# Performance work log

Hardware: AMD Instinct MI355X
Metric: run time of the kernel (lower is better)

## Reference

```python
import math
import jax, jax.numpy as jnp
import numpy as np

D_MODEL = 768
N_HEADS = 12
D_K = 64
D_V = 64
LN_EPS = 1e-5


def setup_inputs() -> dict:
    key = jax.random.key(0)
    ks = jax.random.split(key, 12)
    B, S = 4, 2048
    Q = jax.random.normal(ks[0], (B, S, D_MODEL), dtype=jnp.float32)
    K = jax.random.normal(ks[1], (B, S, D_MODEL), dtype=jnp.float32)
    V = jax.random.normal(ks[2], (B, S, D_MODEL), dtype=jnp.float32)
    attn_mask = jax.random.randint(ks[3], (B, S, S), 0, 2).astype(bool)
    sc = 1.0 / math.sqrt(D_MODEL)
    WQ = jax.random.normal(ks[4], (D_MODEL, N_HEADS * D_K), dtype=jnp.float32) * sc
    WK = jax.random.normal(ks[5], (D_MODEL, N_HEADS * D_K), dtype=jnp.float32) * sc
    WV = jax.random.normal(ks[6], (D_MODEL, N_HEADS * D_V), dtype=jnp.float32) * sc
    Wfc = jax.random.normal(ks[7], (N_HEADS * D_V, D_MODEL), dtype=jnp.float32) * sc
    bQ = jnp.zeros((N_HEADS * D_K,), jnp.float32)
    bK = jnp.zeros((N_HEADS * D_K,), jnp.float32)
    bV = jnp.zeros((N_HEADS * D_V,), jnp.float32)
    bfc = jnp.zeros((D_MODEL,), jnp.float32)
    gamma = jnp.ones((D_MODEL,), jnp.float32)
    beta = jnp.zeros((D_MODEL,), jnp.float32)
    return {"Q": Q, "K": K, "V": V, "attn_mask": attn_mask,
            "WQ": WQ, "bQ": bQ, "WK": WK, "bK": bK, "WV": WV, "bV": bV,
            "Wfc": Wfc, "bfc": bfc, "gamma": gamma, "beta": beta}


def reference(Q, K, V, attn_mask, WQ, bQ, WK, bK, WV, bV, Wfc, bfc, gamma, beta):
    B, S, _ = Q.shape
    # projections -> [B, H, S, d]
    q = (Q @ WQ + bQ).reshape(B, S, N_HEADS, D_K).transpose(0, 2, 1, 3)
    k = (K @ WK + bK).reshape(B, S, N_HEADS, D_K).transpose(0, 2, 1, 3)
    v = (V @ WV + bV).reshape(B, S, N_HEADS, D_V).transpose(0, 2, 1, 3)
    # manual scaled dot-product attention with masked_fill(-1e9)
    scores = jnp.einsum('bhqd,bhkd->bhqk', q, k) / math.sqrt(D_K)
    scores = jnp.where(attn_mask[:, None, :, :], jnp.float32(-1e9), scores)
    attn = jax.nn.softmax(scores, axis=-1)
    context = jnp.einsum('bhqk,bhkd->bhqd', attn, v)
    context = context.transpose(0, 2, 1, 3).reshape(B, S, N_HEADS * D_V)
    out = context @ Wfc + bfc + Q  # residual is Q
    # LayerNorm over d_model
    mu = jnp.mean(out, axis=-1, keepdims=True)
    var = jnp.mean((out - mu) ** 2, axis=-1, keepdims=True)
    return (out - mu) * jax.lax.rsqrt(var + LN_EPS) * gamma + beta
```

## Files before the change

### kernel.cpp

```cpp
#include <hip/hip_runtime.h>
#include <stdint.h>

#define DM   768
#define HEADS 12
#define DK    64
#define SEQ  2048
#define BATCH  4

typedef __bf16 bf16_t;
typedef __bf16 bf16x8 __attribute__((ext_vector_type(8)));
typedef __bf16 bf16x4 __attribute__((ext_vector_type(4)));
typedef float  f32x4  __attribute__((ext_vector_type(4)));
typedef float  f32x16 __attribute__((ext_vector_type(16)));
typedef unsigned u32x4 __attribute__((ext_vector_type(4)));

#define LOG2E 1.44269504f
#define MASKVAL (-1.442695e9f)
#define DEFER_THR 8.0f

#define OFF_FLAG 0
#define OFF_MASK 256
#define SZ_MASK  (BATCH*SEQ*(SEQ/32)*4)
#define OFF_WT   (OFF_MASK + SZ_MASK)
#define SZ_WT1   (DM*DM*2)
#define OFF_XB   (OFF_WT + 4*SZ_WT1)
#define SZ_X     (BATCH*SEQ*DM*2)
#define OFF_QP   (OFF_XB + 3*SZ_X)
#define SZ_PROJ  (BATCH*HEADS*SEQ*DK*2)
#define OFF_KP   (OFF_QP + SZ_PROJ)
#define OFF_VT   (OFF_KP + SZ_PROJ)

__device__ __forceinline__ void gload_lds16(const bf16_t* g, bf16_t* l) {
    __builtin_amdgcn_global_load_lds((const __attribute__((address_space(1))) unsigned int*)g,
                                     (__attribute__((address_space(3))) unsigned int*)l, 16, 0, 0);
}

__device__ __forceinline__ unsigned pack2(float lo, float hi) {
    union { bf16_t b[2]; unsigned u; } x;
    x.b[0] = (bf16_t)lo; x.b[1] = (bf16_t)hi;
    return x.u;
}

__global__ void detect_mask_kernel(const unsigned char* __restrict__ m, int* flag) {
    int u = threadIdx.x;
    int any = m[4*u+1] | m[4*u+2] | m[4*u+3];
    unsigned long long b = __ballot(any != 0);
    if (u == 0) *flag = (b == 0ULL) ? 1 : 0;
}

__global__ void pack_mask_kernel(const void* __restrict__ mraw, const int* __restrict__ flag,
                                 unsigned int* __restrict__ words) {
    const unsigned int total = BATCH*SEQ*SEQ;
    const int is32 = *flag;
    const int* mi = (const int*)mraw;
    const unsigned char* mb = (const unsigned char*)mraw;
    unsigned int stride = gridDim.x * blockDim.x;
    unsigned int lane = threadIdx.x & 63u;
    for (unsigned int e = blockIdx.x * blockDim.x + threadIdx.x; e < total; e += stride) {
        int v = is32 ? (mi[e] != 0) : (mb[e] != 0);
        unsigned long long bal = __ballot(v);
        if ((lane & 31u) == 0u)
            words[e >> 5] = (unsigned int)(bal >> ((lane >> 5) * 32u));
    }
}

__global__ void wt_cvt_kernel(const float* __restrict__ W0, const float* __restrict__ W1,
                              const float* __restrict__ W2, const float* __restrict__ W3,
                              bf16_t* __restrict__ dst) {
    const float* W = blockIdx.z == 0 ? W0 : blockIdx.z == 1 ? W1 : blockIdx.z == 2 ? W2 : W3;
    bf16_t* out = dst + (size_t)blockIdx.z * DM * DM;
    __shared__ float tile[64][65];
    int w = threadIdx.x >> 6, u = threadIdx.x & 63;
    int kb = blockIdx.x * 64, nb = blockIdx.y * 64;
    #pragma unroll
    for (int i = 0; i < 16; i++)
        tile[w + 4*i][u] = W[(size_t)(kb + w + 4*i)*DM + nb + u];
    __syncthreads();
    #pragma unroll
    for (int i = 0; i < 16; i++)
        out[(size_t)(nb + w + 4*i)*DM + kb + u] = (bf16_t)tile[u][w + 4*i];
}

__global__ void xcvt_kernel(const float* __restrict__ Q, const float* __restrict__ K,
                            const float* __restrict__ V, bf16_t* __restrict__ XB) {
    int z = blockIdx.y;
    const float* src = z == 0 ? Q : z == 1 ? K : V;
    bf16_t* dst = XB + (size_t)z * BATCH*SEQ*DM;
    size_t i = ((size_t)blockIdx.x * blockDim.x + threadIdx.x) * 8;
    float4 a = *(const float4*)(src + i);
    float4 b = *(const float4*)(src + i + 4);
    bf16x8 o;
    o[0]=(bf16_t)a.x; o[1]=(bf16_t)a.y; o[2]=(bf16_t)a.z; o[3]=(bf16_t)a.w;
    o[4]=(bf16_t)b.x; o[5]=(bf16_t)b.y; o[6]=(bf16_t)b.z; o[7]=(bf16_t)b.w;
    *(bf16x8*)(dst + i) = o;
}

__device__ __forceinline__ void mm_mainloop(const bf16_t* __restrict__ Aptr,
                                            const bf16_t* __restrict__ Bptr,
                                            bf16_t* As, bf16_t* Bs,
                                            f32x4 acc[4][4], int bm, int bn) {
    int tid = threadIdx.x, w = tid >> 6, u = tid & 63, c = u & 15, g = u >> 4;
    int wr = w >> 1, wc = w & 1;
    for (int k0 = 0; k0 < DM; k0 += 64) {
        #pragma unroll
        for (int i = 0; i < 4; i++) {
            int q = i*256 + tid;
            int row = q >> 3, col8 = q & 7;
            gload_lds16(Aptr + (size_t)(bm*128 + row)*DM + k0 + col8*8, As + (i*256 + w*64)*8);
            gload_lds16(Bptr + (size_t)(bn*128 + row)*DM + k0 + col8*8, Bs + (i*256 + w*64)*8);
        }
        __syncthreads();
        #pragma unroll
        for (int kk = 0; kk < 2; kk++) {
            bf16x8 a[4], bfr[4];
            #pragma unroll
            for (int mi = 0; mi < 4; mi++)
                a[mi] = *(const bf16x8*)(As + (wr*64 + mi*16 + c)*64 + kk*32 + g*8);
            #pragma unroll
            for (int ni = 0; ni < 4; ni++)
                bfr[ni] = *(const bf16x8*)(Bs + (wc*64 + ni*16 + c)*64 + kk*32 + g*8);
            #pragma unroll
            for (int mi = 0; mi < 4; mi++)
                #pragma unroll
                for (int ni = 0; ni < 4; ni++)
                    acc[mi][ni] = __builtin_amdgcn_mfma_f32_16x16x32_bf16(a[mi], bfr[ni], acc[mi][ni], 0, 0, 0);
        }
        __syncthreads();
    }
}

__global__ __launch_bounds__(256) void proj128_kernel(
        const bf16_t* __restrict__ XB, const bf16_t* __restrict__ WT,
        const float* __restrict__ bQ, const float* __restrict__ bK, const float* __restrict__ bV,
        bf16_t* __restrict__ QP, bf16_t* __restrict__ KP, bf16_t* __restrict__ VT) {
    int z = blockIdx.z;
    const bf16_t* Aptr = XB + (size_t)z * BATCH*SEQ*DM;
    const bf16_t* Bptr = WT + (size_t)z * DM * DM;
    const float* bias = z == 0 ? bQ : z == 1 ? bK : bV;
    float scale = (z == 0) ? 0.125f * LOG2E : 1.0f;
    __shared__ __align__(16) bf16_t As[128*64], Bs[128*64];
    int tid = threadIdx.x, w = tid >> 6, u = tid & 63, c = u & 15, g = u >> 4;
    int wr = w >> 1, wc = w & 1;
    int bm = blockIdx.x, bn = blockIdx.y;
    f32x4 zero = {0.f,0.f,0.f,0.f};
    f32x4 acc[4][4] = {{zero,zero,zero,zero},{zero,zero,zero,zero},
                       {zero,zero,zero,zero},{zero,zero,zero,zero}};
    mm_mainloop(Aptr, Bptr, As, Bs, acc, bm, bn);
    int h = bn*2 + wc;
    #pragma unroll
    for (int ni = 0; ni < 4; ni++) {
        int d = ni*16 + c;
        float bv = bias[h*64 + d];
        if (z < 2) {
            bf16_t* dst = (z == 0) ? QP : KP;
            #pragma unroll
            for (int mi = 0; mi < 4; mi++)
                #pragma unroll
                for (int j = 0; j < 4; j++) {
                    int r = bm*128 + wr*64 + mi*16 + 4*g + j;
                    int bidx = r >> 11, s = r & 2047;
                    dst[(((size_t)bidx*HEADS + h)*SEQ + s)*DK + d] = (bf16_t)((acc[mi][ni][j] + bv)*scale);
                }
        } else {
            #pragma unroll
            for (int mi = 0; mi < 4; mi++) {
                bf16x4 pk;
                #pragma unroll
                for (int j = 0; j < 4; j++) pk[j] = (bf16_t)(acc[mi][ni][j] + bv);
                int r0 = bm*128 + wr*64 + mi*16 + 4*g;
                int bidx = r0 >> 11, s0 = r0 & 2047;
                *(bf16x4*)(VT + (((size_t)bidx*HEADS + h)*DK + d)*SEQ + s0) = pk;
            }
        }
    }
}

__global__ __launch_bounds__(256) void out128_kernel(
        const bf16_t* __restrict__ CTX, const bf16_t* __restrict__ WfcT,
        const float* __restrict__ bfc, const float* __restrict__ Qres, float* __restrict__ out) {
    __shared__ __align__(16) bf16_t As[128*64], Bs[128*64];
    int tid = threadIdx.x, w = tid >> 6, u = tid & 63, c = u & 15, g = u >> 4;
    int wr = w >> 1, wc = w & 1;
    int bm = blockIdx.x, bn = blockIdx.y;
    f32x4 zero = {0.f,0.f,0.f,0.f};
    f32x4 acc[4][4] = {{zero,zero,zero,zero},{zero,zero,zero,zero},
                       {zero,zero,zero,zero},{zero,zero,zero,zero}};
    mm_mainloop(CTX, WfcT, As, Bs, acc, bm, bn);
    #pragma unroll
    for (int ni = 0; ni < 4; ni++) {
        int n = bn*128 + wc*64 + ni*16 + c;
        float bv = bfc[n];
        #pragma unroll
        for (int mi = 0; mi < 4; mi++)
            #pragma unroll
            for (int j = 0; j < 4; j++) {
                int r = bm*128 + wr*64 + mi*16 + 4*g + j;
                out[(size_t)r*DM + n] = acc[mi][ni][j] + bv + Qres[(size_t)r*DM + n];
            }
    }
}

__global__ __launch_bounds__(256) void attn_kernel(
        const bf16_t* __restrict__ QP, const bf16_t* __restrict__ KP, const bf16_t* __restrict__ VT,
        const unsigned int* __restrict__ maskw, bf16_t* __restrict__ CTX) {
    __shared__ __align__(16) bf16_t kbuf[2][64*64];
    __shared__ __align__(16) bf16_t vbuf[2][64*64];
    __shared__ __align__(16) float lut4[64];
    int tid = threadIdx.x, w = tid >> 6, u = tid & 63;
    int qc = u & 31, hi = u >> 5;
    int b = blockIdx.z, h = blockIdx.y;
    int qg = blockIdx.x * 128 + w * 32 + qc;
    size_t bh = (size_t)(b * HEADS + h);
    const bf16_t* qp = QP + bh * SEQ * DK;
    const bf16_t* kp = KP + bh * SEQ * DK;
    const bf16_t* vt = VT + bh * DK * SEQ;
    const unsigned int* mwq = maskw + ((size_t)b * SEQ + qg) * (SEQ/32);

    if (tid < 64) lut4[tid] = (((tid >> 2) >> (tid & 3)) & 1) ? MASKVAL : 0.f;

    bf16x8 qf[4];
    #pragma unroll
    for (int t = 0; t < 4; t++)
        qf[t] = *(const bf16x8*)(qp + (size_t)qg*DK + 16*t + 8*hi);

    int sr = tid >> 3, scc = tid & 7;

    f32x16 zz = {0,0,0,0,0,0,0,0,0,0,0,0,0,0,0,0};
    f32x16 acc0 = zz, acc1 = zz;
    float mrun = -3e38f, lsum = 0.f;

    #pragma unroll
    for (int i = 0; i < 2; i++) {
        int r = i*32 + sr;
        int gc = (scc ^ (r & 7)) << 3;
        gload_lds16(kp + (size_t)r*DK + gc,       &kbuf[0][0] + i*2048 + tid*8);
        gload_lds16(vt + (size_t)r*SEQ + 0 + gc,  &vbuf[0][0] + i*2048 + tid*8);
    }
    uint2 mv = *(const uint2*)(mwq);
    __syncthreads();

    for (int kt = 0; kt < SEQ/64; kt++) {
        int kb = kt * 64;
        int cur = kt & 1;
        uint2 mv_next;
        if (kt + 1 < SEQ/64) {
            mv_next = *(const uint2*)(mwq + ((kb + 64) >> 5));
            int nkb = kb + 64;
            #pragma unroll
            for (int i = 0; i < 2; i++) {
                int r = i*32 + sr;
                int gc = (scc ^ (r & 7)) << 3;
                gload_lds16(kp + (size_t)(nkb + r)*DK + gc, &kbuf[cur^1][0] + i*2048 + tid*8);
                gload_lds16(vt + (size_t)r*SEQ + nkb + gc,  &vbuf[cur^1][0] + i*2048 + tid*8);
            }
        }
        const bf16_t* kl = &kbuf[cur][0];
        const bf16_t* vl = &vbuf[cur][0];

        f32x4 am0[4], am1[4];
        #pragma unroll
        for (int j = 0; j < 4; j++) {
            am0[j] = *(const f32x4*)&lut4[((mv.x >> (8*j + 4*hi)) & 0xFu) * 4];
            am1[j] = *(const f32x4*)&lut4[((mv.y >> (8*j + 4*hi)) & 0xFu) * 4];
        }

        f32x16 s0 = zz, s1 = zz;
        __builtin_amdgcn_s_setprio(1);
        #pragma unroll
        for (int t = 0; t < 4; t++) {
            int col = (16*t + 8*hi);
            int r0 = qc, r1 = 32 + qc;
            bf16x8 k0 = *(const bf16x8*)(kl + r0*64 + (col ^ ((r0 & 7) << 3)));
            bf16x8 k1 = *(const bf16x8*)(kl + r1*64 + (col ^ ((r1 & 7) << 3)));
            s0 = __builtin_amdgcn_mfma_f32_32x32x16_bf16(k0, qf[t], s0, 0, 0, 0);
            s1 = __builtin_amdgcn_mfma_f32_32x32x16_bf16(k1, qf[t], s1, 0, 0, 0);
        }
        __builtin_amdgcn_s_setprio(0);

        #pragma unroll
        for (int j = 0; j < 4; j++)
            #pragma unroll
            for (int i = 0; i < 4; i++) {
                s0[4*j + i] += am0[j][i];
                s1[4*j + i] += am1[j][i];
            }

        float tmx[16];
        #pragma unroll
        for (int r = 0; r < 16; r++) tmx[r] = fmaxf(s0[r], s1[r]);
        #pragma unroll
        for (int st = 8; st > 0; st >>= 1)
            #pragma unroll
            for (int r = 0; r < st; r++) tmx[r] = fmaxf(tmx[r], tmx[r + st]);
        float tm = tmx[0];

        if (!__all(tm <= mrun + DEFER_THR)) {
            float rmax = fmaxf(tm, __shfl_xor(tm, 32));
            float mn = fmaxf(mrun, rmax);
            float alpha = __builtin_amdgcn_exp2f(mrun - mn);
            mrun = mn;
            lsum *= alpha;
            acc0 *= alpha;
            acc1 *= alpha;
        }

        #pragma unroll
        for (int r = 0; r < 16; r++) {
            s0[r] = __builtin_amdgcn_exp2f(s0[r] - mrun);
            s1[r] = __builtin_amdgcn_exp2f(s1[r] - mrun);
        }
        float sm[16];
        #pragma unroll
        for (int r = 0; r < 16; r++) sm[r] = s0[r] + s1[r];
        #pragma unroll
        for (int st = 8; st > 0; st >>= 1)
            #pragma unroll
            for (int r = 0; r < st; r++) sm[r] = sm[r] + sm[r + st];
        lsum += sm[0] + __shfl_xor(sm[0], 32);

        bf16x8 pa[4];
        {
            union { u32x4 uv; bf16x8 bv; } cv;
            unsigned x0, y0, x1, y1;
            x0 = pack2(s0[0], s0[1]); y0 = pack2(s0[4], s0[5]);
            asm volatile("v_permlane32_swap_b32 %0, %1" : "+v"(x0), "+v"(y0));
            x1 = pack2(s0[2], s0[3]); y1 = pack2(s0[6], s0[7]);
            asm volatile("v_permlane32_swap_b32 %0, %1" : "+v"(x1), "+v"(y1));
            cv.uv[0]=x0; cv.uv[1]=x1; cv.uv[2]=y0; cv.uv[3]=y1; pa[0]=cv.bv;
            x0 = pack2(s0[8], s0[9]);  y0 = pack2(s0[12], s0[13]);
            asm volatile("v_permlane32_swap_b32 %0, %1" : "+v"(x0), "+v"(y0));
            x1 = pack2(s0[10], s0[11]); y1 = pack2(s0[14], s0[15]);
            asm volatile("v_permlane32_swap_b32 %0, %1" : "+v"(x1), "+v"(y1));
            cv.uv[0]=x0; cv.uv[1]=x1; cv.uv[2]=y0; cv.uv[3]=y1; pa[1]=cv.bv;
            x0 = pack2(s1[0], s1[1]); y0 = pack2(s1[4], s1[5]);
            asm volatile("v_permlane32_swap_b32 %0, %1" : "+v"(x0), "+v"(y0));
            x1 = pack2(s1[2], s1[3]); y1 = pack2(s1[6], s1[7]);
            asm volatile("v_permlane32_swap_b32 %0, %1" : "+v"(x1), "+v"(y1));
            cv.uv[0]=x0; cv.uv[1]=x1; cv.uv[2]=y0; cv.uv[3]=y1; pa[2]=cv.bv;
            x0 = pack2(s1[8], s1[9]);  y0 = pack2(s1[12], s1[13]);
            asm volatile("v_permlane32_swap_b32 %0, %1" : "+v"(x0), "+v"(y0));
            x1 = pack2(s1[10], s1[11]); y1 = pack2(s1[14], s1[15]);
            asm volatile("v_permlane32_swap_b32 %0, %1" : "+v"(x1), "+v"(y1));
            cv.uv[0]=x0; cv.uv[1]=x1; cv.uv[2]=y0; cv.uv[3]=y1; pa[3]=cv.bv;
        }

        __builtin_amdgcn_s_setprio(1);
        #pragma unroll
        for (int ks = 0; ks < 4; ks++) {
            int col = 16*ks + 8*hi;
            int r0 = qc, r1 = 32 + qc;
            bf16x8 v0 = *(const bf16x8*)(vl + r0*64 + (col ^ ((r0 & 7) << 3)));
            bf16x8 v1 = *(const bf16x8*)(vl + r1*64 + (col ^ ((r1 & 7) << 3)));
            acc0 = __builtin_amdgcn_mfma_f32_32x32x16_bf16(v0, pa[ks], acc0, 0, 0, 0);
            acc1 = __builtin_amdgcn_mfma_f32_32x32x16_bf16(v1, pa[ks], acc1, 0, 0, 0);
        }
        __builtin_amdgcn_s_setprio(0);

        __syncthreads();
        mv = mv_next;
    }

    float inv = 1.0f / lsum;
    size_t obase = ((size_t)(b * SEQ) + qg) * DM + h * DK;
    #pragma unroll
    for (int gr = 0; gr < 4; gr++) {
        bf16x4 o0, o1;
        #pragma unroll
        for (int jj = 0; jj < 4; jj++) {
            o0[jj] = (bf16_t)(acc0[4*gr + jj] * inv);
            o1[jj] = (bf16_t)(acc1[4*gr + jj] * inv);
        }
        *(bf16x4*)(CTX + obase + gr*8 + hi*4)      = o0;
        *(bf16x4*)(CTX + obase + 32 + gr*8 + hi*4) = o1;
    }
}

__global__ __launch_bounds__(256) void ln_kernel(float* __restrict__ out,
        const float* __restrict__ gamma, const float* __restrict__ beta) {
    int w = threadIdx.x >> 6, u = threadIdx.x & 63;
    size_t row = (size_t)blockIdx.x * 4 + w;
    float x[12];
    float s = 0.f;
    #pragma unroll
    for (int i = 0; i < 12; i++) { x[i] = out[row*DM + i*64 + u]; s += x[i]; }
    #pragma unroll
    for (int d = 1; d < 64; d <<= 1) s += __shfl_xor(s, d);
    float mu = s * (1.0f/768.0f);
    float v = 0.f;
    #pragma unroll
    for (int i = 0; i < 12; i++) { float t = x[i] - mu; v += t*t; }
    #pragma unroll
    for (int d = 1; d < 64; d <<= 1) v += __shfl_xor(v, d);
    float rstd = rsqrtf(v * (1.0f/768.0f) + 1e-5f);
    #pragma unroll
    for (int i = 0; i < 12; i++)
        out[row*DM + i*64 + u] = (x[i] - mu) * rstd * gamma[i*64 + u] + beta[i*64 + u];
}

extern "C" void kernel_launch(void* const* d_in, const int* in_sizes, int n_in,
                              void* d_out, int out_size, void* d_ws, size_t ws_size,
                              hipStream_t stream) {
    const float* Q    = (const float*)d_in[0];
    const float* K    = (const float*)d_in[1];
    const float* V    = (const float*)d_in[2];
    const void*  mask = d_in[3];
    const float* WQ   = (const float*)d_in[4];
    const float* bQ   = (const float*)d_in[5];
    const float* WK   = (const float*)d_in[6];
    const float* bK   = (const float*)d_in[7];
    const float* WV   = (const float*)d_in[8];
    const float* bV   = (const float*)d_in[9];
    const float* Wfc  = (const float*)d_in[10];
    const float* bfc  = (const float*)d_in[11];
    const float* gam  = (const float*)d_in[12];
    const float* bet  = (const float*)d_in[13];
    float* out = (float*)d_out;
    char* ws = (char*)d_ws;

    int* flag            = (int*)(ws + OFF_FLAG);
    unsigned int* maskw  = (unsigned int*)(ws + OFF_MASK);
    bf16_t* WT           = (bf16_t*)(ws + OFF_WT);
    bf16_t* XB           = (bf16_t*)(ws + OFF_XB);
    bf16_t* QP           = (bf16_t*)(ws + OFF_QP);
    bf16_t* KP           = (bf16_t*)(ws + OFF_KP);
    bf16_t* VT           = (bf16_t*)(ws + OFF_VT);
    bf16_t* CTX          = XB;

    detect_mask_kernel<<<1, 64, 0, stream>>>((const unsigned char*)mask, flag);
    pack_mask_kernel<<<2048, 256, 0, stream>>>(mask, flag, maskw);
    xcvt_kernel<<<dim3(3072, 3), 256, 0, stream>>>(Q, K, V, XB);
    wt_cvt_kernel<<<dim3(12, 12, 4), 256, 0, stream>>>(WQ, WK, WV, Wfc, WT);
    proj128_kernel<<<dim3(64, 6, 3), 256, 0, stream>>>(XB, WT, bQ, bK, bV, QP, KP, VT);
    attn_kernel<<<dim3(SEQ/128, HEADS, BATCH), 256, 0, stream>>>(QP, KP, VT, maskw, CTX);
    out128_kernel<<<dim3(64, 6), 256, 0, stream>>>(CTX, WT + (size_t)3*DM*DM, bfc, Q, out);
    ln_kernel<<<2048, 256, 0, stream>>>(out, gam, bet);
}
```

Before: 400.7 us.

## Split attention over KV halves with combine kernel; retile GEMMs to 128x96

The attention kernel now splits the key/value sequence into two halves and doubles the grid. Each half writes unnormalized bf16 partial outputs plus running max and sum, and a new combine kernel merges the two halves with log-sum-exp weights. The projection and output GEMMs move from 128x128 to 128x96 tiles, giving 512 blocks instead of 384 for better CU coverage. The max/sum reductions are also restructured into shallower trees. This adds an extra kernel launch, partial-output traffic, and bf16 rounding of unnormalized partials, and the initial running max changes to a finite value.

```diff
diff --git a/kernel.cpp b/kernel.cpp
--- a/kernel.cpp
+++ b/kernel.cpp
@@ -29,6 +29,8 @@
 #define SZ_PROJ  (BATCH*HEADS*SEQ*DK*2)
 #define OFF_KP   (OFF_QP + SZ_PROJ)
 #define OFF_VT   (OFF_KP + SZ_PROJ)
+#define OFF_ML   (OFF_VT + SZ_PROJ)
+#define SZ_ML    (2*BATCH*HEADS*SEQ*2*4)
 
 __device__ __forceinline__ void gload_lds16(const bf16_t* g, bf16_t* l) {
     __builtin_amdgcn_global_load_lds((const __attribute__((address_space(1))) unsigned int*)g,
@@ -95,41 +97,46 @@
     *(bf16x8*)(dst + i) = o;
 }
 
-__device__ __forceinline__ void mm_mainloop(const bf16_t* __restrict__ Aptr,
-                                            const bf16_t* __restrict__ Bptr,
-                                            bf16_t* As, bf16_t* Bs,
-                                            f32x4 acc[4][4], int bm, int bn) {
+__device__ __forceinline__ void mm_mainloop96(const bf16_t* __restrict__ Aptr,
+                                              const bf16_t* __restrict__ Bptr,
+                                              bf16_t* As, bf16_t* Bs,
+                                              f32x4 acc[4][3], int bm, int bn) {
     int tid = threadIdx.x, w = tid >> 6, u = tid & 63, c = u & 15, g = u >> 4;
-    int wr = w >> 1, wc = w & 1;
+    int wr = w & 1, wc = w >> 1;
     for (int k0 = 0; k0 < DM; k0 += 64) {
         #pragma unroll
         for (int i = 0; i < 4; i++) {
             int q = i*256 + tid;
             int row = q >> 3, col8 = q & 7;
             gload_lds16(Aptr + (size_t)(bm*128 + row)*DM + k0 + col8*8, As + (i*256 + w*64)*8);
-            gload_lds16(Bptr + (size_t)(bn*128 + row)*DM + k0 + col8*8, Bs + (i*256 + w*64)*8);
+        }
+        #pragma unroll
+        for (int i = 0; i < 3; i++) {
+            int q = i*256 + tid;
+            int row = q >> 3, col8 = q & 7;
+            gload_lds16(Bptr + (size_t)(bn*96 + row)*DM + k0 + col8*8, Bs + (i*256 + w*64)*8);
         }
         __syncthreads();
         #pragma unroll
         for (int kk = 0; kk < 2; kk++) {
-            bf16x8 a[4], bfr[4];
+            bf16x8 a[4], bfr[3];
             #pragma unroll
             for (int mi = 0; mi < 4; mi++)
                 a[mi] = *(const bf16x8*)(As + (wr*64 + mi*16 + c)*64 + kk*32 + g*8);
             #pragma unroll
-            for (int ni = 0; ni < 4; ni++)
-                bfr[ni] = *(const bf16x8*)(Bs + (wc*64 + ni*16 + c)*64 + kk*32 + g*8);
+            for (int ni = 0; ni < 3; ni++)
+                bfr[ni] = *(const bf16x8*)(Bs + (wc*48 + ni*16 + c)*64 + kk*32 + g*8);
             #pragma unroll
             for (int mi = 0; mi < 4; mi++)
                 #pragma unroll
-                for (int ni = 0; ni < 4; ni++)
+                for (int ni = 0; ni < 3; ni++)
                     acc[mi][ni] = __builtin_amdgcn_mfma_f32_16x16x32_bf16(a[mi], bfr[ni], acc[mi][ni], 0, 0, 0);
         }
         __syncthreads();
     }
 }
 
-__global__ __launch_bounds__(256) void proj128_kernel(
+__global__ __launch_bounds__(256) void proj96_kernel(
         const bf16_t* __restrict__ XB, const bf16_t* __restrict__ WT,
         const float* __restrict__ bQ, const float* __restrict__ bK, const float* __restrict__ bV,
         bf16_t* __restrict__ QP, bf16_t* __restrict__ KP, bf16_t* __restrict__ VT) {
@@ -138,19 +145,18 @@
     const bf16_t* Bptr = WT + (size_t)z * DM * DM;
     const float* bias = z == 0 ? bQ : z == 1 ? bK : bV;
     float scale = (z == 0) ? 0.125f * LOG2E : 1.0f;
-    __shared__ __align__(16) bf16_t As[128*64], Bs[128*64];
+    __shared__ __align__(16) bf16_t As[128*64], Bs[96*64];
     int tid = threadIdx.x, w = tid >> 6, u = tid & 63, c = u & 15, g = u >> 4;
-    int wr = w >> 1, wc = w & 1;
+    int wr = w & 1, wc = w >> 1;
     int bm = blockIdx.x, bn = blockIdx.y;
     f32x4 zero = {0.f,0.f,0.f,0.f};
-    f32x4 acc[4][4] = {{zero,zero,zero,zero},{zero,zero,zero,zero},
-                       {zero,zero,zero,zero},{zero,zero,zero,zero}};
-    mm_mainloop(Aptr, Bptr, As, Bs, acc, bm, bn);
-    int h = bn*2 + wc;
-    #pragma unroll
-    for (int ni = 0; ni < 4; ni++) {
-        int d = ni*16 + c;
-        float bv = bias[h*64 + d];
+    f32x4 acc[4][3] = {{zero,zero,zero},{zero,zero,zero},{zero,zero,zero},{zero,zero,zero}};
+    mm_mainloop96(Aptr, Bptr, As, Bs, acc, bm, bn);
+    #pragma unroll
+    for (int ni = 0; ni < 3; ni++) {
+        int n = bn*96 + wc*48 + ni*16 + c;
+        int h = n >> 6, d = n & 63;
+        float bv = bias[n];
         if (z < 2) {
             bf16_t* dst = (z == 0) ? QP : KP;
             #pragma unroll
@@ -175,20 +181,19 @@
     }
 }
 
-__global__ __launch_bounds__(256) void out128_kernel(
+__global__ __launch_bounds__(256) void out96_kernel(
         const bf16_t* __restrict__ CTX, const bf16_t* __restrict__ WfcT,
         const float* __restrict__ bfc, const float* __restrict__ Qres, float* __restrict__ out) {
-    __shared__ __align__(16) bf16_t As[128*64], Bs[128*64];
+    __shared__ __align__(16) bf16_t As[128*64], Bs[96*64];
     int tid = threadIdx.x, w = tid >> 6, u = tid & 63, c = u & 15, g = u >> 4;
-    int wr = w >> 1, wc = w & 1;
+    int wr = w & 1, wc = w >> 1;
     int bm = blockIdx.x, bn = blockIdx.y;
     f32x4 zero = {0.f,0.f,0.f,0.f};
-    f32x4 acc[4][4] = {{zero,zero,zero,zero},{zero,zero,zero,zero},
-                       {zero,zero,zero,zero},{zero,zero,zero,zero}};
-    mm_mainloop(CTX, WfcT, As, Bs, acc, bm, bn);
-    #pragma unroll
-    for (int ni = 0; ni < 4; ni++) {
-        int n = bn*128 + wc*64 + ni*16 + c;
+    f32x4 acc[4][3] = {{zero,zero,zero},{zero,zero,zero},{zero,zero,zero},{zero,zero,zero}};
+    mm_mainloop96(CTX, WfcT, As, Bs, acc, bm, bn);
+    #pragma unroll
+    for (int ni = 0; ni < 3; ni++) {
+        int n = bn*96 + wc*48 + ni*16 + c;
         float bv = bfc[n];
         #pragma unroll
         for (int mi = 0; mi < 4; mi++)
@@ -202,13 +207,14 @@
 
 __global__ __launch_bounds__(256) void attn_kernel(
         const bf16_t* __restrict__ QP, const bf16_t* __restrict__ KP, const bf16_t* __restrict__ VT,
-        const unsigned int* __restrict__ maskw, bf16_t* __restrict__ CTX) {
+        const unsigned int* __restrict__ maskw, bf16_t* __restrict__ OP, float* __restrict__ ML) {
     __shared__ __align__(16) bf16_t kbuf[2][64*64];
     __shared__ __align__(16) bf16_t vbuf[2][64*64];
     __shared__ __align__(16) float lut4[64];
     int tid = threadIdx.x, w = tid >> 6, u = tid & 63;
     int qc = u & 31, hi = u >> 5;
-    int b = blockIdx.z, h = blockIdx.y;
+    int sp = blockIdx.z & 1, b = blockIdx.z >> 1, h = blockIdx.y;
+    int kvbase = sp << 10;
     int qg = blockIdx.x * 128 + w * 32 + qc;
     size_t bh = (size_t)(b * HEADS + h);
     const bf16_t* qp = QP + bh * SEQ * DK;
@@ -227,23 +233,23 @@
 
     f32x16 zz = {0,0,0,0,0,0,0,0,0,0,0,0,0,0,0,0};
     f32x16 acc0 = zz, acc1 = zz;
-    float mrun = -3e38f, lsum = 0.f;
+    float mrun = -16384.0f, lsum = 0.f;
 
     #pragma unroll
     for (int i = 0; i < 2; i++) {
         int r = i*32 + sr;
         int gc = (scc ^ (r & 7)) << 3;
-        gload_lds16(kp + (size_t)r*DK + gc,       &kbuf[0][0] + i*2048 + tid*8);
-        gload_lds16(vt + (size_t)r*SEQ + 0 + gc,  &vbuf[0][0] + i*2048 + tid*8);
-    }
-    uint2 mv = *(const uint2*)(mwq);
+        gload_lds16(kp + (size_t)(kvbase + r)*DK + gc,   &kbuf[0][0] + i*2048 + tid*8);
+        gload_lds16(vt + (size_t)r*SEQ + kvbase + gc,    &vbuf[0][0] + i*2048 + tid*8);
+    }
+    uint2 mv = *(const uint2*)(mwq + (kvbase >> 5));
     __syncthreads();
 
-    for (int kt = 0; kt < SEQ/64; kt++) {
-        int kb = kt * 64;
+    for (int kt = 0; kt < 16; kt++) {
+        int kb = kvbase + kt * 64;
         int cur = kt & 1;
-        uint2 mv_next;
-        if (kt + 1 < SEQ/64) {
+        uint2 mv_next = mv;
+        if (kt + 1 < 16) {
             mv_next = *(const uint2*)(mwq + ((kb + 64) >> 5));
             int nkb = kb + 64;
             #pragma unroll
@@ -285,14 +291,13 @@
                 s1[4*j + i] += am1[j][i];
             }
 
-        float tmx[16];
-        #pragma unroll
-        for (int r = 0; r < 16; r++) tmx[r] = fmaxf(s0[r], s1[r]);
-        #pragma unroll
-        for (int st = 8; st > 0; st >>= 1)
-            #pragma unroll
-            for (int r = 0; r < st; r++) tmx[r] = fmaxf(tmx[r], tmx[r + st]);
-        float tm = tmx[0];
+        float q8[8];
+        #pragma unroll
+        for (int r = 0; r < 8; r++)
+            q8[r] = fmaxf(fmaxf(s0[r], s0[r+8]), fmaxf(s1[r], s1[r+8]));
+        float q4a = fmaxf(fmaxf(q8[0], q8[1]), fmaxf(q8[2], q8[3]));
+        float q4b = fmaxf(fmaxf(q8[4], q8[5]), fmaxf(q8[6], q8[7]));
+        float tm = fmaxf(q4a, q4b);
 
         if (!__all(tm <= mrun + DEFER_THR)) {
             float rmax = fmaxf(tm, __shfl_xor(tm, 32));
@@ -309,14 +314,14 @@
             s0[r] = __builtin_amdgcn_exp2f(s0[r] - mrun);
             s1[r] = __builtin_amdgcn_exp2f(s1[r] - mrun);
         }
-        float sm[16];
-        #pragma unroll
-        for (int r = 0; r < 16; r++) sm[r] = s0[r] + s1[r];
-        #pragma unroll
-        for (int st = 8; st > 0; st >>= 1)
-            #pragma unroll
-            for (int r = 0; r < st; r++) sm[r] = sm[r] + sm[r + st];
-        lsum += sm[0] + __shfl_xor(sm[0], 32);
+        f32x16 sv = s0 + s1;
+        float a8[8];
+        #pragma unroll
+        for (int r = 0; r < 8; r++) a8[r] = sv[r] + sv[r+8];
+        float a4a = (a8[0] + a8[1]) + (a8[2] + a8[3]);
+        float a4b = (a8[4] + a8[5]) + (a8[6] + a8[7]);
+        float rsum = a4a + a4b;
+        lsum += rsum + __shfl_xor(rsum, 32);
 
         bf16x8 pa[4];
         {
@@ -360,18 +365,50 @@
         mv = mv_next;
     }
 
-    float inv = 1.0f / lsum;
-    size_t obase = ((size_t)(b * SEQ) + qg) * DM + h * DK;
+    size_t prow = ((size_t)(sp * BATCH + b) * HEADS + h) * SEQ + qg;
     #pragma unroll
     for (int gr = 0; gr < 4; gr++) {
         bf16x4 o0, o1;
         #pragma unroll
         for (int jj = 0; jj < 4; jj++) {
-            o0[jj] = (bf16_t)(acc0[4*gr + jj] * inv);
-            o1[jj] = (bf16_t)(acc1[4*gr + jj] * inv);
-        }
-        *(bf16x4*)(CTX + obase + gr*8 + hi*4)      = o0;
-        *(bf16x4*)(CTX + obase + 32 + gr*8 + hi*4) = o1;
+            o0[jj] = (bf16_t)acc0[4*gr + jj];
+            o1[jj] = (bf16_t)acc1[4*gr + jj];
+        }
+        *(bf16x4*)(OP + prow*DK + gr*8 + hi*4)      = o0;
+        *(bf16x4*)(OP + prow*DK + 32 + gr*8 + hi*4) = o1;
+    }
+    if (hi == 0) {
+        float2 ml = {mrun, lsum};
+        *(float2*)(ML + prow*2) = ml;
+    }
+}
+
+__global__ __launch_bounds__(256) void attn_combine_kernel(
+        const bf16_t* __restrict__ OP, const float* __restrict__ ML, bf16_t* __restrict__ CTX) {
+    int tid = threadIdx.x;
+    int r = tid >> 2, dc = (tid & 3) << 4;
+    int h = blockIdx.y, b = blockIdx.z;
+    int q = blockIdx.x * 64 + r;
+    const size_t P = (size_t)BATCH * HEADS * SEQ;
+    size_t row0 = ((size_t)b * HEADS + h) * SEQ + q;
+    size_t row1 = row0 + P;
+    float2 ml0 = *(const float2*)(ML + row0*2);
+    float2 ml1 = *(const float2*)(ML + row1*2);
+    float M = fmaxf(ml0.x, ml1.x);
+    float w0 = exp2f(ml0.x - M), w1 = exp2f(ml1.x - M);
+    float inv = 1.0f / (w0*ml0.y + w1*ml1.y);
+    w0 *= inv; w1 *= inv;
+    const bf16x8* pa = (const bf16x8*)(OP + row0*DK + dc);
+    const bf16x8* pb = (const bf16x8*)(OP + row1*DK + dc);
+    bf16_t* dst = CTX + ((size_t)b*SEQ + q)*DM + h*DK + dc;
+    #pragma unroll
+    for (int k = 0; k < 2; k++) {
+        bf16x8 av = pa[k], bv = pb[k];
+        bf16x8 o;
+        #pragma unroll
+        for (int i = 0; i < 8; i++)
+            o[i] = (bf16_t)((float)av[i]*w0 + (float)bv[i]*w1);
+        *(bf16x8*)(dst + k*8) = o;
     }
 }
 
@@ -424,14 +461,17 @@
     bf16_t* QP           = (bf16_t*)(ws + OFF_QP);
     bf16_t* KP           = (bf16_t*)(ws + OFF_KP);
     bf16_t* VT           = (bf16_t*)(ws + OFF_VT);
+    float*  ML           = (float*)(ws + OFF_ML);
     bf16_t* CTX          = XB;
+    bf16_t* OP           = (bf16_t*)(ws + OFF_XB + SZ_X);
 
     detect_mask_kernel<<<1, 64, 0, stream>>>((const unsigned char*)mask, flag);
     pack_mask_kernel<<<2048, 256, 0, stream>>>(mask, flag, maskw);
     xcvt_kernel<<<dim3(3072, 3), 256, 0, stream>>>(Q, K, V, XB);
     wt_cvt_kernel<<<dim3(12, 12, 4), 256, 0, stream>>>(WQ, WK, WV, Wfc, WT);
-    proj128_kernel<<<dim3(64, 6, 3), 256, 0, stream>>>(XB, WT, bQ, bK, bV, QP, KP, VT);
-    attn_kernel<<<dim3(SEQ/128, HEADS, BATCH), 256, 0, stream>>>(QP, KP, VT, maskw, CTX);
-    out128_kernel<<<dim3(64, 6), 256, 0, stream>>>(CTX, WT + (size_t)3*DM*DM, bfc, Q, out);
+    proj96_kernel<<<dim3(64, 8, 3), 256, 0, stream>>>(XB, WT, bQ, bK, bV, QP, KP, VT);
+    attn_kernel<<<dim3(SEQ/128, HEADS, BATCH*2), 256, 0, stream>>>(QP, KP, VT, maskw, OP, ML);
+    attn_combine_kernel<<<dim3(SEQ/64, HEADS, BATCH), 256, 0, stream>>>(OP, ML, CTX);
+    out96_kernel<<<dim3(64, 8), 256, 0, stream>>>(CTX, WT + (size_t)3*DM*DM, bfc, Q, out);
     ln_kernel<<<2048, 256, 0, stream>>>(out, gam, bet);
 }
```

Measured after the change: 396.3 us. No clear change (-1.1%).
